# Kernel tuning notes

Measured on AMD Instinct MI355X. Metric: run time of the kernel, lower is better.

## Reference

```python
import jax, jax.numpy as jnp
import numpy as np

NUM_INTERNAL = 4000
MAX_CHILDREN = 16
BATCH = 1024


def _build_tree():
    # Deterministic synthetic hierarchy: child counts in [2, 16].
    counts = 2 + (np.arange(NUM_INTERNAL) * 7) % 15
    row = np.repeat(np.arange(NUM_INTERNAL), counts)
    col = np.concatenate([np.arange(n) for n in counts])
    flat_index = row * MAX_CHILDREN + col          # scatter slots in padded buffer
    num_nodes = int(counts.sum()) + 1              # +1 for the root
    child_index = np.arange(1, num_nodes)          # every non-root node is a child once
    return flat_index, child_index, num_nodes


def setup_inputs() -> dict:
    flat_index, child_index, num_nodes = _build_tree()
    key = jax.random.key(0)
    scores = jax.random.normal(key, (BATCH, flat_index.shape[0]), dtype=jnp.float32)
    return {
        "scores": scores,
        "flat_index": jnp.asarray(flat_index, dtype=jnp.int32),
        "child_index": jnp.asarray(child_index, dtype=jnp.int32),
        "num_internal": NUM_INTERNAL,
        "max_num_children": MAX_CHILDREN,
        "num_nodes": num_nodes,
    }


def reference(scores, flat_index, child_index, num_internal, max_num_children, num_nodes):
    lead = scores.shape[:-1]
    neg_inf = jnp.asarray(-jnp.inf, scores.dtype)
    # Scatter scores into padded [num_internal, max_num_children] buffer (-inf padding).
    flat = jnp.full((*lead, num_internal * max_num_children), neg_inf, dtype=scores.dtype)
    flat = flat.at[..., flat_index].set(scores)
    # Per-internal-node (grouped) log-softmax over the padded child axis.
    child_log_p = jax.nn.log_softmax(
        flat.reshape(*lead, num_internal, max_num_children), axis=-1
    ).reshape(*lead, num_internal * max_num_children)
    # Gather real slots back and scatter into node-indexed output (root stays 0).
    out = jnp.zeros((*lead, num_nodes), dtype=scores.dtype)
    out = out.at[..., child_index].set(child_log_p[..., flat_index])
    return out


if __name__ == "__main__":
    inp = setup_inputs()
    y = reference(**inp)
    print(y.shape, y.dtype)
```

## Files before the change

### kernel.cpp

```cpp
#include <hip/hip_runtime.h>
#include <math.h>

#define MAXC  16
#define GPB   256
#define BLOCK 256
#define ROWS  8
#define CAP   2464

__global__ void build_offs_kernel(const int* __restrict__ flat_index,
                                  const int* __restrict__ p_num_internal,
                                  const int* __restrict__ p_max_children,
                                  int n_scores,
                                  int* __restrict__ offs) {
    int j = blockIdx.x * blockDim.x + threadIdx.x;
    int mc = p_max_children[0];
    if (j < n_scores) {
        int fi = flat_index[j];
        int g  = fi / mc;
        if (fi - g * mc == 0) offs[g] = j;
    }
    if (j == 0) offs[p_num_internal[0]] = n_scores;
}

__device__ __forceinline__ void bar_lds() {
    asm volatile("s_waitcnt lgkmcnt(0)" ::: "memory");
    __builtin_amdgcn_s_barrier();
    asm volatile("" ::: "memory");
}

__global__ void __launch_bounds__(BLOCK)
hier_logsoftmax_kernel(const float* __restrict__ scores,
                       const int* __restrict__ offs,
                       const int* __restrict__ p_num_internal,
                       float* __restrict__ out,
                       int n_scores, int num_nodes, int batch) {
    __shared__ __align__(16) float lbuf[CAP];
    __shared__ float dump[BLOCK];

    const int ni      = p_num_internal[0];
    const int nchunks = (ni + GPB - 1) / GPB;
    const int tid     = (int)threadIdx.x;
    const int b0      = (int)blockIdx.y * ROWS;
    if (b0 >= batch) return;
    const int nrows = min(ROWS, batch - b0);

    for (int chunk = (int)blockIdx.x; chunk < nchunks; chunk += (int)gridDim.x) {
        const int g0   = chunk * GPB;
        const int gend = min(g0 + GPB, ni);
        const int e0   = offs[g0];
        const int n    = offs[gend] - e0;
        const int d    = e0 & 3;

        const int hL  = min(n, (4 - (e0 & 3)) & 3);
        const int nvL = (n - hL) >> 2;
        const int tL  = n - hL - 4 * nvL;

        const int A0  = 1 + e0;
        const int hS  = min(n, (4 - (A0 & 3)) & 3);
        const int nvS = (n - hS) >> 2;
        const int tS  = n - hS - 4 * nvS;
        const int B0  = (d + hS) >> 2;

        const int g = g0 + tid;
        int lo = 0, c = 0;
        if (g < gend) {
            const int og = offs[g];
            c  = offs[g + 1] - og;
            lo = d + (og - e0);
        }

        const int  i0 = hL + 4 * tid;
        const int  i1 = i0 + 4 * BLOCK;
        const int  i2 = i1 + 4 * BLOCK;
        const bool q0 = tid < nvL, q1 = tid + BLOCK < nvL, q2 = tid + 2 * BLOCK < nvL;
        const int  it = hL + 4 * nvL + tid;
        const bool qh = tid < hL, qt = tid < tL;

        const float* sr = scores + (size_t)b0 * n_scores + e0;
        float4 r0, r1, r2;
        float  rh = 0.f, rt = 0.f;
        if (q0) r0 = *(const float4*)(sr + i0);
        if (q1) r1 = *(const float4*)(sr + i1);
        if (q2) r2 = *(const float4*)(sr + i2);
        if (qh) rh = sr[tid];
        if (qt) rt = sr[it];

        for (int rr = 0; rr < nrows; ++rr) {
            float* __restrict__ orow = out + (size_t)(b0 + rr) * num_nodes;

            if (q0) *(float4*)&lbuf[d + i0] = r0;
            if (q1) *(float4*)&lbuf[d + i1] = r1;
            if (q2) *(float4*)&lbuf[d + i2] = r2;
            if (qh) lbuf[d + tid] = rh;
            if (qt) lbuf[d + it]  = rt;
            bar_lds();

            if (rr + 1 < nrows) {
                const float* s2 = scores + (size_t)(b0 + rr + 1) * n_scores + e0;
                if (q0) r0 = *(const float4*)(s2 + i0);
                if (q1) r1 = *(const float4*)(s2 + i1);
                if (q2) r2 = *(const float4*)(s2 + i2);
                if (qh) rh = s2[tid];
                if (qt) rt = s2[it];
            }

            if (g < gend) {
                float v[MAXC];
                #pragma unroll
                for (int k = 0; k < MAXC; ++k)
                    v[k] = (k < c) ? lbuf[lo + k] : -INFINITY;
                float m = v[0];
                #pragma unroll
                for (int k = 1; k < MAXC; ++k) m = fmaxf(m, v[k]);
                float s0 = 0.f, s1 = 0.f;
                #pragma unroll
                for (int k = 0; k < MAXC; k += 2) {
                    s0 += __expf(v[k] - m);
                    s1 += __expf(v[k + 1] - m);
                }
                const float lse = m + __logf(s0 + s1);
                #pragma unroll
                for (int k = 0; k < MAXC; ++k) {
                    float* p = (k < c) ? &lbuf[lo + k] : &dump[tid];
                    *p = v[k] - lse;
                }
            }
            bar_lds();

            for (int p = tid; p < nvS; p += BLOCK) {
                const float  x   = lbuf[4 * (B0 + p) + 3];
                const float4 blk = *(const float4*)&lbuf[4 * (B0 + p + 1)];
                float4 t; t.x = x; t.y = blk.x; t.z = blk.y; t.w = blk.z;
                *(float4*)&orow[A0 + hS + 4 * p] = t;
            }
            if (tid < hS) orow[A0 + tid] = lbuf[d + tid];
            if (tid < tS) {
                const int j = hS + 4 * nvS + tid;
                orow[A0 + j] = lbuf[d + j];
            }
            if (chunk == 0 && tid == 0) orow[0] = 0.0f;
            bar_lds();
        }
    }
}

extern "C" void kernel_launch(void* const* d_in, const int* in_sizes, int n_in,
                              void* d_out, int out_size, void* d_ws, size_t ws_size,
                              hipStream_t stream) {
    const float* scores     = (const float*)d_in[0];
    const int*   flat_index = (const int*)d_in[1];
    const int*   p_ni       = (const int*)d_in[3];
    const int*   p_mc       = (const int*)d_in[4];

    const int n_scores  = in_sizes[1];
    const int batch     = in_sizes[0] / n_scores;
    const int num_nodes = out_size / batch;

    int* offs = (int*)d_ws;

    {
        dim3 blk(256), grd((n_scores + 255) / 256);
        hipLaunchKernelGGL(build_offs_kernel, grd, blk, 0, stream,
                           flat_index, p_ni, p_mc, n_scores, offs);
    }

    {
        dim3 blk(BLOCK), grd(16, (batch + ROWS - 1) / ROWS);
        hipLaunchKernelGGL(hier_logsoftmax_kernel, grd, blk, 0, stream,
                           scores, offs, p_ni, out_size ? (float*)d_out : (float*)d_out,
                           n_scores, num_nodes, batch);
    }
}
```

Before: 276.1 us.

## Transpose LDS child layout via precomputed index maps and double-buffer rows

Precomputes 16-bit LDS scatter/gather addresses per score so each group's children sit in a strided pair-interleaved layout, letting each thread read its children as float2 with few bank conflicts instead of contiguous per-thread spans. Double-buffers LDS by row parity to remove one barrier per row, halves ROWS to 4 for more blocks, and uses nontemporal output stores. The cost is extra index loads and scalar LDS scatter/gather, plus more LDS usage.

Result: no change. 271.3 us (-1.8%).

```diff
diff --git a/kernel.cpp b/kernel.cpp
--- a/kernel.cpp
+++ b/kernel.cpp
@@ -3,23 +3,33 @@
 
 #define MAXC  16
 #define GPB   256
+#define GPBP  259
+#define PAIRS (MAXC / 2)
+#define BUFSZ 4160
 #define BLOCK 256
-#define ROWS  8
-#define CAP   2464
-
-__global__ void build_offs_kernel(const int* __restrict__ flat_index,
-                                  const int* __restrict__ p_num_internal,
-                                  const int* __restrict__ p_max_children,
+#define ROWS  4
+
+typedef float f32x4 __attribute__((ext_vector_type(4)));
+
+__global__ void build_meta_kernel(const int* __restrict__ flat_index,
+                                  const int* __restrict__ p_ni,
+                                  const int* __restrict__ p_mc,
                                   int n_scores,
-                                  int* __restrict__ offs) {
+                                  int* __restrict__ offs,
+                                  unsigned short* __restrict__ a16a,
+                                  unsigned short* __restrict__ a16b) {
     int j = blockIdx.x * blockDim.x + threadIdx.x;
-    int mc = p_max_children[0];
+    int mc = p_mc[0];
     if (j < n_scores) {
-        int fi = flat_index[j];
-        int g  = fi / mc;
-        if (fi - g * mc == 0) offs[g] = j;
-    }
-    if (j == 0) offs[p_num_internal[0]] = n_scores;
+        int fi  = flat_index[j];
+        int g   = fi / mc;
+        int col = fi - g * mc;
+        if (col == 0) offs[g] = j;
+        unsigned short a = (unsigned short)((col >> 1) * (2 * GPBP) + 2 * g + (col & 1));
+        a16a[j]     = a;
+        a16b[j + 1] = a;
+    }
+    if (j == 0) { offs[p_ni[0]] = n_scores; a16b[0] = 0; }
 }
 
 __device__ __forceinline__ void bar_lds() {
@@ -31,13 +41,14 @@
 __global__ void __launch_bounds__(BLOCK)
 hier_logsoftmax_kernel(const float* __restrict__ scores,
                        const int* __restrict__ offs,
-                       const int* __restrict__ p_num_internal,
+                       const unsigned short* __restrict__ a16a,
+                       const unsigned short* __restrict__ a16b,
+                       const int* __restrict__ p_ni,
                        float* __restrict__ out,
                        int n_scores, int num_nodes, int batch) {
-    __shared__ __align__(16) float lbuf[CAP];
-    __shared__ float dump[BLOCK];
-
-    const int ni      = p_num_internal[0];
+    __shared__ __align__(16) float lbuf[2 * BUFSZ];
+
+    const int ni      = p_ni[0];
     const int nchunks = (ni + GPB - 1) / GPB;
     const int tid     = (int)threadIdx.x;
     const int b0      = (int)blockIdx.y * ROWS;
@@ -49,25 +60,19 @@
         const int gend = min(g0 + GPB, ni);
         const int e0   = offs[g0];
         const int n    = offs[gend] - e0;
-        const int d    = e0 & 3;
+        const int g2   = 2 * g0;
 
         const int hL  = min(n, (4 - (e0 & 3)) & 3);
         const int nvL = (n - hL) >> 2;
         const int tL  = n - hL - 4 * nvL;
-
         const int A0  = 1 + e0;
         const int hS  = min(n, (4 - (A0 & 3)) & 3);
         const int nvS = (n - hS) >> 2;
         const int tS  = n - hS - 4 * nvS;
-        const int B0  = (d + hS) >> 2;
 
         const int g = g0 + tid;
-        int lo = 0, c = 0;
-        if (g < gend) {
-            const int og = offs[g];
-            c  = offs[g + 1] - og;
-            lo = d + (og - e0);
-        }
+        int c = 0;
+        if (g < gend) c = offs[g + 1] - offs[g];
 
         const int  i0 = hL + 4 * tid;
         const int  i1 = i0 + 4 * BLOCK;
@@ -76,9 +81,25 @@
         const int  it = hL + 4 * nvL + tid;
         const bool qh = tid < hL, qt = tid < tL;
 
+        ushort4 ua0, ua1, ua2; unsigned short ah = 0, at = 0;
+        if (q0) ua0 = *(const ushort4*)&a16a[e0 + i0];
+        if (q1) ua1 = *(const ushort4*)&a16a[e0 + i1];
+        if (q2) ua2 = *(const ushort4*)&a16a[e0 + i2];
+        if (qh) ah = a16a[e0 + tid];
+        if (qt) at = a16a[e0 + it];
+
+        const int  s0 = tid, s1 = tid + BLOCK, s2 = tid + 2 * BLOCK;
+        const bool p0 = s0 < nvS, p1 = s1 < nvS, p2 = s2 < nvS;
+        ushort4 ub0, ub1, ub2; unsigned short bh = 0, bt = 0;
+        if (p0) ub0 = *(const ushort4*)&a16b[e0 + hS + 4 * s0 + 1];
+        if (p1) ub1 = *(const ushort4*)&a16b[e0 + hS + 4 * s1 + 1];
+        if (p2) ub2 = *(const ushort4*)&a16b[e0 + hS + 4 * s2 + 1];
+        if (tid < hS) bh = a16a[e0 + tid];
+        const int jt = hS + 4 * nvS + tid;
+        if (tid < tS) bt = a16a[e0 + jt];
+
         const float* sr = scores + (size_t)b0 * n_scores + e0;
-        float4 r0, r1, r2;
-        float  rh = 0.f, rt = 0.f;
+        float4 r0, r1, r2; float rh = 0.f, rt = 0.f;
         if (q0) r0 = *(const float4*)(sr + i0);
         if (q1) r1 = *(const float4*)(sr + i1);
         if (q2) r2 = *(const float4*)(sr + i2);
@@ -87,59 +108,73 @@
 
         for (int rr = 0; rr < nrows; ++rr) {
             float* __restrict__ orow = out + (size_t)(b0 + rr) * num_nodes;
-
-            if (q0) *(float4*)&lbuf[d + i0] = r0;
-            if (q1) *(float4*)&lbuf[d + i1] = r1;
-            if (q2) *(float4*)&lbuf[d + i2] = r2;
-            if (qh) lbuf[d + tid] = rh;
-            if (qt) lbuf[d + it]  = rt;
+            const int bo = (rr & 1) ? BUFSZ : 0;
+
+            if (q0) { lbuf[bo + (int)ua0.x - g2] = r0.x; lbuf[bo + (int)ua0.y - g2] = r0.y;
+                      lbuf[bo + (int)ua0.z - g2] = r0.z; lbuf[bo + (int)ua0.w - g2] = r0.w; }
+            if (q1) { lbuf[bo + (int)ua1.x - g2] = r1.x; lbuf[bo + (int)ua1.y - g2] = r1.y;
+                      lbuf[bo + (int)ua1.z - g2] = r1.z; lbuf[bo + (int)ua1.w - g2] = r1.w; }
+            if (q2) { lbuf[bo + (int)ua2.x - g2] = r2.x; lbuf[bo + (int)ua2.y - g2] = r2.y;
+                      lbuf[bo + (int)ua2.z - g2] = r2.z; lbuf[bo + (int)ua2.w - g2] = r2.w; }
+            if (qh) lbuf[bo + (int)ah - g2] = rh;
+            if (qt) lbuf[bo + (int)at - g2] = rt;
+
+            if (rr + 1 < nrows) {
+                const float* s2p = scores + (size_t)(b0 + rr + 1) * n_scores + e0;
+                if (q0) r0 = *(const float4*)(s2p + i0);
+                if (q1) r1 = *(const float4*)(s2p + i1);
+                if (q2) r2 = *(const float4*)(s2p + i2);
+                if (qh) rh = s2p[tid];
+                if (qt) rt = s2p[it];
+            }
             bar_lds();
 
-            if (rr + 1 < nrows) {
-                const float* s2 = scores + (size_t)(b0 + rr + 1) * n_scores + e0;
-                if (q0) r0 = *(const float4*)(s2 + i0);
-                if (q1) r1 = *(const float4*)(s2 + i1);
-                if (q2) r2 = *(const float4*)(s2 + i2);
-                if (qh) rh = s2[tid];
-                if (qt) rt = s2[it];
-            }
-
             if (g < gend) {
+                float2 v2[PAIRS];
+                #pragma unroll
+                for (int jp = 0; jp < PAIRS; ++jp)
+                    v2[jp] = *(const float2*)&lbuf[bo + jp * (2 * GPBP) + 2 * tid];
                 float v[MAXC];
                 #pragma unroll
-                for (int k = 0; k < MAXC; ++k)
-                    v[k] = (k < c) ? lbuf[lo + k] : -INFINITY;
+                for (int jp = 0; jp < PAIRS; ++jp) {
+                    v[2 * jp]     = (2 * jp     < c) ? v2[jp].x : -INFINITY;
+                    v[2 * jp + 1] = (2 * jp + 1 < c) ? v2[jp].y : -INFINITY;
+                }
                 float m = v[0];
                 #pragma unroll
                 for (int k = 1; k < MAXC; ++k) m = fmaxf(m, v[k]);
-                float s0 = 0.f, s1 = 0.f;
+                float sa = 0.f, sb = 0.f;
                 #pragma unroll
                 for (int k = 0; k < MAXC; k += 2) {
-                    s0 += __expf(v[k] - m);
-                    s1 += __expf(v[k + 1] - m);
+                    sa += __expf(v[k] - m);
+                    sb += __expf(v[k + 1] - m);
                 }
-                const float lse = m + __logf(s0 + s1);
-                #pragma unroll
-                for (int k = 0; k < MAXC; ++k) {
-                    float* p = (k < c) ? &lbuf[lo + k] : &dump[tid];
-                    *p = v[k] - lse;
+                const float lse = m + __logf(sa + sb);
+                #pragma unroll
+                for (int jp = 0; jp < PAIRS; ++jp) {
+                    float2 w;
+                    w.x = v[2 * jp] - lse;
+                    w.y = v[2 * jp + 1] - lse;
+                    *(float2*)&lbuf[bo + jp * (2 * GPBP) + 2 * tid] = w;
                 }
             }
             bar_lds();
 
-            for (int p = tid; p < nvS; p += BLOCK) {
-                const float  x   = lbuf[4 * (B0 + p) + 3];
-                const float4 blk = *(const float4*)&lbuf[4 * (B0 + p + 1)];
-                float4 t; t.x = x; t.y = blk.x; t.z = blk.y; t.w = blk.z;
-                *(float4*)&orow[A0 + hS + 4 * p] = t;
-            }
-            if (tid < hS) orow[A0 + tid] = lbuf[d + tid];
-            if (tid < tS) {
-                const int j = hS + 4 * nvS + tid;
-                orow[A0 + j] = lbuf[d + j];
-            }
+            if (p0) { f32x4 t;
+                      t.x = lbuf[bo + (int)ub0.x - g2]; t.y = lbuf[bo + (int)ub0.y - g2];
+                      t.z = lbuf[bo + (int)ub0.z - g2]; t.w = lbuf[bo + (int)ub0.w - g2];
+                      __builtin_nontemporal_store(t, (f32x4*)&orow[A0 + hS + 4 * s0]); }
+            if (p1) { f32x4 t;
+                      t.x = lbuf[bo + (int)ub1.x - g2]; t.y = lbuf[bo + (int)ub1.y - g2];
+                      t.z = lbuf[bo + (int)ub1.z - g2]; t.w = lbuf[bo + (int)ub1.w - g2];
+                      __builtin_nontemporal_store(t, (f32x4*)&orow[A0 + hS + 4 * s1]); }
+            if (p2) { f32x4 t;
+                      t.x = lbuf[bo + (int)ub2.x - g2]; t.y = lbuf[bo + (int)ub2.y - g2];
+                      t.z = lbuf[bo + (int)ub2.z - g2]; t.w = lbuf[bo + (int)ub2.w - g2];
+                      __builtin_nontemporal_store(t, (f32x4*)&orow[A0 + hS + 4 * s2]); }
+            if (tid < hS) orow[A0 + tid] = lbuf[bo + (int)bh - g2];
+            if (tid < tS) orow[A0 + jt]  = lbuf[bo + (int)bt - g2];
             if (chunk == 0 && tid == 0) orow[0] = 0.0f;
-            bar_lds();
         }
     }
 }
@@ -156,18 +191,24 @@
     const int batch     = in_sizes[0] / n_scores;
     const int num_nodes = out_size / batch;
 
-    int* offs = (int*)d_ws;
+    char* ws = (char*)d_ws;
+    int* offs = (int*)ws;
+    size_t off_a = ((size_t)(n_scores + 2) * 4 + 255) & ~(size_t)255;
+    unsigned short* a16a = (unsigned short*)(ws + off_a);
+    size_t off_b = off_a + (((size_t)(n_scores + 8) * 2 + 255) & ~(size_t)255);
+    unsigned short* a16b = (unsigned short*)(ws + off_b);
+    float* out = (float*)d_out;
 
     {
         dim3 blk(256), grd((n_scores + 255) / 256);
-        hipLaunchKernelGGL(build_offs_kernel, grd, blk, 0, stream,
-                           flat_index, p_ni, p_mc, n_scores, offs);
+        hipLaunchKernelGGL(build_meta_kernel, grd, blk, 0, stream,
+                           flat_index, p_ni, p_mc, n_scores, offs, a16a, a16b);
     }
 
     {
         dim3 blk(BLOCK), grd(16, (batch + ROWS - 1) / ROWS);
         hipLaunchKernelGGL(hier_logsoftmax_kernel, grd, blk, 0, stream,
-                           scores, offs, p_ni, out_size ? (float*)d_out : (float*)d_out,
+                           scores, offs, a16a, a16b, p_ni, out,
                            n_scores, num_nodes, batch);
     }
 }
```

## Stream score rows into LDS via async global_load_lds triple buffering

Applied to the files above, without the earlier changes.

Replaces the register-staged row prefetch with direct global-to-LDS DMA loads into three rotating tiles, letting the load of upcoming rows overlap the softmax and store of the current row, synchronised with explicit vmcnt waits. It also halves the rows per block (8 to 4), which doubles the grid height, and turns the branchy edge stores into predicated writes that go to a global dump buffer instead of skipping. This raises parallelism and removes the VGPR staging, at the cost of hand-counted vmcnt values that must match the number of outstanding loads. It also adds extra redundant global writes to the dump area.

Result: no change. 271.2 us (-1.8%).

```diff
diff --git a/kernel.cpp b/kernel.cpp
--- a/kernel.cpp
+++ b/kernel.cpp
@@ -4,22 +4,30 @@
 #define MAXC  16
 #define GPB   256
 #define BLOCK 256
-#define ROWS  8
-#define CAP   2464
+#define ROWS  4
+#define TILE_INSTR 12
+#define TILE_F (TILE_INSTR * 256)
+#define NBUF  3
+#define DUMPF (NBUF * TILE_F)
+#define LDS_F (DUMPF + 256 + 64)
+
+typedef float f32x4 __attribute__((ext_vector_type(4)));
+
+#define VMCNT(N) asm volatile("s_waitcnt vmcnt(" #N ")" ::: "memory")
 
 __global__ void build_offs_kernel(const int* __restrict__ flat_index,
-                                  const int* __restrict__ p_num_internal,
-                                  const int* __restrict__ p_max_children,
+                                  const int* __restrict__ p_ni,
+                                  const int* __restrict__ p_mc,
                                   int n_scores,
                                   int* __restrict__ offs) {
     int j = blockIdx.x * blockDim.x + threadIdx.x;
-    int mc = p_max_children[0];
+    int mc = p_mc[0];
     if (j < n_scores) {
         int fi = flat_index[j];
         int g  = fi / mc;
         if (fi - g * mc == 0) offs[g] = j;
     }
-    if (j == 0) offs[p_num_internal[0]] = n_scores;
+    if (j == 0) offs[p_ni[0]] = n_scores;
 }
 
 __device__ __forceinline__ void bar_lds() {
@@ -28,83 +36,63 @@
     asm volatile("" ::: "memory");
 }
 
+__device__ __forceinline__ void dma16(const float* g, float* l) {
+    __builtin_amdgcn_global_load_lds(
+        (const __attribute__((address_space(1))) unsigned int*)g,
+        (__attribute__((address_space(3))) unsigned int*)l,
+        16, 0, 0);
+}
+
 __global__ void __launch_bounds__(BLOCK)
 hier_logsoftmax_kernel(const float* __restrict__ scores,
                        const int* __restrict__ offs,
-                       const int* __restrict__ p_num_internal,
+                       const int* __restrict__ p_ni,
                        float* __restrict__ out,
+                       float* __restrict__ dump,
                        int n_scores, int num_nodes, int batch) {
-    __shared__ __align__(16) float lbuf[CAP];
-    __shared__ float dump[BLOCK];
-
-    const int ni      = p_num_internal[0];
+    __shared__ __align__(16) float lbuf[LDS_F];
+
+    const int ni      = p_ni[0];
     const int nchunks = (ni + GPB - 1) / GPB;
     const int tid     = (int)threadIdx.x;
+    const int wid     = tid >> 6;
+    const int lane    = tid & 63;
     const int b0      = (int)blockIdx.y * ROWS;
     if (b0 >= batch) return;
     const int nrows = min(ROWS, batch - b0);
+    const int fmax  = batch * n_scores - 4;
+    float* __restrict__ dumpg = dump + (((int)blockIdx.y & 63) << 8);
 
     for (int chunk = (int)blockIdx.x; chunk < nchunks; chunk += (int)gridDim.x) {
         const int g0   = chunk * GPB;
         const int gend = min(g0 + GPB, ni);
         const int e0   = offs[g0];
         const int n    = offs[gend] - e0;
-        const int d    = e0 & 3;
-
-        const int hL  = min(n, (4 - (e0 & 3)) & 3);
-        const int nvL = (n - hL) >> 2;
-        const int tL  = n - hL - 4 * nvL;
-
-        const int A0  = 1 + e0;
-        const int hS  = min(n, (4 - (A0 & 3)) & 3);
-        const int nvS = (n - hS) >> 2;
-        const int tS  = n - hS - 4 * nvS;
-        const int B0  = (d + hS) >> 2;
 
         const int g = g0 + tid;
-        int lo = 0, c = 0;
-        if (g < gend) {
-            const int og = offs[g];
-            c  = offs[g + 1] - og;
-            lo = d + (og - e0);
-        }
-
-        const int  i0 = hL + 4 * tid;
-        const int  i1 = i0 + 4 * BLOCK;
-        const int  i2 = i1 + 4 * BLOCK;
-        const bool q0 = tid < nvL, q1 = tid + BLOCK < nvL, q2 = tid + 2 * BLOCK < nvL;
-        const int  it = hL + 4 * nvL + tid;
-        const bool qh = tid < hL, qt = tid < tL;
-
-        const float* sr = scores + (size_t)b0 * n_scores + e0;
-        float4 r0, r1, r2;
-        float  rh = 0.f, rt = 0.f;
-        if (q0) r0 = *(const float4*)(sr + i0);
-        if (q1) r1 = *(const float4*)(sr + i1);
-        if (q2) r2 = *(const float4*)(sr + i2);
-        if (qh) rh = sr[tid];
-        if (qt) rt = sr[it];
-
-        for (int rr = 0; rr < nrows; ++rr) {
-            float* __restrict__ orow = out + (size_t)(b0 + rr) * num_nodes;
-
-            if (q0) *(float4*)&lbuf[d + i0] = r0;
-            if (q1) *(float4*)&lbuf[d + i1] = r1;
-            if (q2) *(float4*)&lbuf[d + i2] = r2;
-            if (qh) lbuf[d + tid] = rh;
-            if (qt) lbuf[d + it]  = rt;
-            bar_lds();
-
-            if (rr + 1 < nrows) {
-                const float* s2 = scores + (size_t)(b0 + rr + 1) * n_scores + e0;
-                if (q0) r0 = *(const float4*)(s2 + i0);
-                if (q1) r1 = *(const float4*)(s2 + i1);
-                if (q2) r2 = *(const float4*)(s2 + i2);
-                if (qh) rh = s2[tid];
-                if (qt) rt = s2[it];
-            }
+        int lo_base = 0, c = 0;
+        if (g < gend) { int og = offs[g]; c = offs[g + 1] - og; lo_base = og - e0; }
+
+        auto issue_row = [&](int rr, int bufF) {
+            const int rab  = b0 + rr;
+            const int Rb   = rab * n_scores + e0;
+            const int src0 = Rb & ~3;
+            #pragma unroll
+            for (int k = 0; k < 3; ++k) {
+                const int iid  = wid * 3 + k;
+                int fidx = src0 + iid * 256 + lane * 4;
+                fidx = min(fidx, fmax);
+                const int loff = __builtin_amdgcn_readfirstlane(bufF + iid * 256);
+                dma16(scores + fidx, &lbuf[loff]);
+            }
+        };
+
+        auto process = [&](int rr, int bufF) {
+            const int rab   = b0 + rr;
+            const int shift = (rab * n_scores + e0) & 3;
 
             if (g < gend) {
+                const int lo = bufF + shift + lo_base;
                 float v[MAXC];
                 #pragma unroll
                 for (int k = 0; k < MAXC; ++k)
@@ -112,34 +100,90 @@
                 float m = v[0];
                 #pragma unroll
                 for (int k = 1; k < MAXC; ++k) m = fmaxf(m, v[k]);
-                float s0 = 0.f, s1 = 0.f;
+                float sa = 0.f, sb = 0.f;
                 #pragma unroll
                 for (int k = 0; k < MAXC; k += 2) {
-                    s0 += __expf(v[k] - m);
-                    s1 += __expf(v[k + 1] - m);
+                    sa += __expf(v[k] - m);
+                    sb += __expf(v[k + 1] - m);
                 }
-                const float lse = m + __logf(s0 + s1);
+                const float lse = m + __logf(sa + sb);
                 #pragma unroll
                 for (int k = 0; k < MAXC; ++k) {
-                    float* p = (k < c) ? &lbuf[lo + k] : &dump[tid];
-                    *p = v[k] - lse;
+                    const int idx = (k < c) ? (lo + k) : (DUMPF + tid);
+                    lbuf[idx] = v[k] - lse;
                 }
             }
             bar_lds();
 
-            for (int p = tid; p < nvS; p += BLOCK) {
-                const float  x   = lbuf[4 * (B0 + p) + 3];
-                const float4 blk = *(const float4*)&lbuf[4 * (B0 + p + 1)];
-                float4 t; t.x = x; t.y = blk.x; t.z = blk.y; t.w = blk.z;
-                *(float4*)&orow[A0 + hS + 4 * p] = t;
-            }
-            if (tid < hS) orow[A0 + tid] = lbuf[d + tid];
-            if (tid < tS) {
-                const int j = hS + 4 * nvS + tid;
-                orow[A0 + j] = lbuf[d + j];
-            }
-            if (chunk == 0 && tid == 0) orow[0] = 0.0f;
-            bar_lds();
+            float* __restrict__ op = out + (size_t)rab * (size_t)num_nodes + 1 + e0;
+            const int al  = (int)(((size_t)rab * (size_t)num_nodes + 1 + e0) & 3);
+            const int hS  = (4 - al) & 3;
+            const int nvS = (n - hS) >> 2;
+            const int tS  = n - hS - 4 * nvS;
+            const int rot = (shift + hS) & 3;
+            const int bq  = bufF + (((shift + hS) >> 2) << 2);
+
+            #define SLOT(S, R) { \
+                const int sp = tid + (S) * 256; \
+                const float4 ta = *(const float4*)&lbuf[bq + 4 * sp]; \
+                const float4 tb = *(const float4*)&lbuf[bq + 4 * sp + 4]; \
+                f32x4 t; \
+                if      ((R) == 0) { t.x = ta.x; t.y = ta.y; t.z = ta.z; t.w = ta.w; } \
+                else if ((R) == 1) { t.x = ta.y; t.y = ta.z; t.z = ta.w; t.w = tb.x; } \
+                else if ((R) == 2) { t.x = ta.z; t.y = ta.w; t.z = tb.x; t.w = tb.y; } \
+                else               { t.x = ta.w; t.y = tb.x; t.z = tb.y; t.w = tb.z; } \
+                f32x4* dst = (sp < nvS) ? (f32x4*)(op + hS + 4 * sp) \
+                                        : (f32x4*)(dumpg + 4 * lane); \
+                *dst = t; }
+
+            switch (rot) {
+                case 0:  SLOT(0,0) SLOT(1,0) SLOT(2,0) break;
+                case 1:  SLOT(0,1) SLOT(1,1) SLOT(2,1) break;
+                case 2:  SLOT(0,2) SLOT(1,2) SLOT(2,2) break;
+                default: SLOT(0,3) SLOT(1,3) SLOT(2,3) break;
+            }
+            #undef SLOT
+            {
+                const float hv = lbuf[bufF + shift + tid];
+                float* dst = (tid < hS) ? (op + tid) : (dumpg + lane);
+                *dst = hv;
+            }
+            {
+                const int jt = hS + 4 * nvS + tid;
+                const float tv = lbuf[bufF + shift + jt];
+                float* dst = (tid < tS) ? (op + jt) : (dumpg + lane);
+                *dst = tv;
+            }
+            {
+                float* dst = (chunk == 0 && tid == 0)
+                           ? (out + (size_t)rab * (size_t)num_nodes) : (dumpg + lane);
+                *dst = 0.0f;
+            }
+        };
+
+        VMCNT(0);
+        bar_lds();
+
+        if (nrows == ROWS) {
+            issue_row(0, 0);
+            issue_row(1, TILE_F);
+            VMCNT(3);  bar_lds();
+            issue_row(2, 2 * TILE_F);
+            process(0, 0);
+            VMCNT(9);  bar_lds();
+            issue_row(3, 0);
+            process(1, TILE_F);
+            VMCNT(15); bar_lds();
+            process(2, 2 * TILE_F);
+            VMCNT(12); bar_lds();
+            process(3, 0);
+        } else {
+            for (int rr = 0; rr < nrows; ++rr) {
+                VMCNT(0); bar_lds();
+                issue_row(rr, 0);
+                VMCNT(0); bar_lds();
+                process(rr, 0);
+            }
         }
     }
 }
@@ -156,7 +200,11 @@
     const int batch     = in_sizes[0] / n_scores;
     const int num_nodes = out_size / batch;
 
-    int* offs = (int*)d_ws;
+    char* ws   = (char*)d_ws;
+    int*  offs = (int*)ws;
+    size_t off_d = ((size_t)(n_scores + 2) * 4 + 255) & ~(size_t)255;
+    float* dump  = (float*)(ws + off_d);
+    float* out   = (float*)d_out;
 
     {
         dim3 blk(256), grd((n_scores + 255) / 256);
@@ -167,7 +215,7 @@
     {
         dim3 blk(BLOCK), grd(16, (batch + ROWS - 1) / ROWS);
         hipLaunchKernelGGL(hier_logsoftmax_kernel, grd, blk, 0, stream,
-                           scores, offs, p_ni, out_size ? (float*)d_out : (float*)d_out,
+                           scores, offs, p_ni, out, dump,
                            n_scores, num_nodes, batch);
     }
 }
```
